# Optimization experiments

Measured on AMD Instinct MI355X. Metric: run time of the kernel, lower is better.

## Reference

```python
import jax, jax.numpy as jnp
import numpy as np

OPTION_NUM = 5
HEADS = 4
NUM_LAYERS = 3
N_NODES = 20000
N_EDGES = 640000
NODES_PER_GRAPH = 800
N_GRAPHS = 25          # N_NODES // NODES_PER_GRAPH, multiple of OPTION_NUM
N_GROUPS = 5           # N_GRAPHS // OPTION_NUM; must equal OPTION_NUM for output_layer
T_TOK = 256
TOKEN_DIM = 1024
D = 256                # out_channels
VOCAB = 100000


def setup_inputs() -> dict:
    key = jax.random.key(0)
    ks = jax.random.split(key, 16)
    nrm = lambda k, s: jax.random.normal(k, s, dtype=jnp.float32) * 0.05
    L = NUM_LAYERS
    return {
        "concept_ids": jax.random.randint(ks[0], (N_NODES,), 0, VOCAB, dtype=jnp.int32),
        "edge_index": jax.random.randint(ks[1], (2, N_EDGES), 0, N_NODES, dtype=jnp.int32),
        "edge_type": jax.random.randint(ks[2], (N_EDGES,), 0, 38, dtype=jnp.int32),
        "sentence_embeddings": nrm(ks[3], (N_GROUPS, TOKEN_DIM)),
        "token_embedding": nrm(ks[4], (N_GROUPS, T_TOK, TOKEN_DIM)),
        "batch": (jnp.arange(N_NODES, dtype=jnp.int32) // NODES_PER_GRAPH),
        "entity_embeddings": nrm(ks[5], (VOCAB, D)),
        "Wq": nrm(ks[6], (L, D, D)), "bq": jnp.zeros((L, D), jnp.float32),
        "Wk": nrm(ks[7], (L, D, D)), "bk": jnp.zeros((L, D), jnp.float32),
        "Wv": nrm(ks[8], (L, D, D)), "bv": jnp.zeros((L, D), jnp.float32),
        "Ws": nrm(ks[9], (L, TOKEN_DIM, D)), "bs": jnp.zeros((L, D), jnp.float32),
        "Wo": nrm(ks[10], (L, D, D)), "bo": jnp.zeros((L, D), jnp.float32),
        "W1": nrm(ks[11], (D, D)), "b1": jnp.zeros((D,), jnp.float32),
        "W2": nrm(ks[12], (TOKEN_DIM, D)), "b2": jnp.zeros((D,), jnp.float32),
        "W3": nrm(ks[13], (D, TOKEN_DIM)), "b3": jnp.zeros((TOKEN_DIM,), jnp.float32),
        "Wout": nrm(ks[14], (OPTION_NUM * D, D)), "bout": jnp.zeros((D,), jnp.float32),
    }


def reference(concept_ids, edge_index, edge_type, sentence_embeddings, token_embedding,
              batch, entity_embeddings, Wq, bq, Wk, bk, Wv, bv, Ws, bs, Wo, bo,
              W1, b1, W2, b2, W3, b3, Wout, bout):
    H = HEADS
    C = D // H
    sqdk = jnp.sqrt(jnp.float32(C))
    group = batch // OPTION_NUM                      # [N] in [0, N_GROUPS)
    row, col = edge_index[0], edge_index[1]

    x = entity_embeddings[concept_ids]               # [N, D]
    for l in range(NUM_LAYERS):
        Q = (x @ Wq[l] + bq[l]).reshape(-1, H, C)
        K = (x @ Wk[l] + bk[l]).reshape(-1, H, C)
        V = (x @ Wv[l] + bv[l]).reshape(-1, H, C)
        QS = (sentence_embeddings[group] @ Ws[l] + bs[l]).reshape(-1, H, C)
        Qi, Kj = Q[row], K[col]                      # [E, H, C]
        alpha = ((Qi * Kj).sum(-1) + (QS[row] * Kj).sum(-1) + (Qi * QS[col]).sum(-1)) / (3.0 * sqdk)
        alpha = jax.nn.leaky_relu(alpha, 0.2)
        alpha = jax.nn.softmax(alpha, axis=0)        # global softmax over edges (as in source)
        agg = jnp.zeros_like(V).at[row].add(V[col] * alpha[:, :, None])
        x = agg.reshape(-1, H * C) @ Wo[l] + bo[l] + x

    x = x @ W1 + b1                                  # [N, D]
    tok = token_embedding @ W2 + b2                  # [G, T, D]

    # attention_multihead (faithful double gather by group indices)
    scale = jnp.sqrt(jnp.float32(D))
    scores = jnp.einsum('nd,btd->bnt', x, tok) / scale   # [G, N, T]
    sel = scores[:, group, :]                            # gather dim 1
    w = jax.nn.softmax(sel, axis=-1)
    ao = jnp.einsum('bnt,btd->bnd', w, tok)              # [G, N, D]
    sel2 = ao[:, group, :]                               # second gather
    concat = jnp.transpose(sel2, (1, 0, 2)).reshape(x.shape[0], -1)  # [N, G*D]
    x = concat @ Wout + bout                             # [N, D]

    pooled = jax.ops.segment_max(x, batch, num_segments=N_GRAPHS)    # global_max_pool
    soft = pooled @ W3 + b3                              # [N_GRAPHS, token_dim]
    return soft.reshape(N_GRAPHS // OPTION_NUM, OPTION_NUM, -1)
```

## Files before the change

### kernel.cpp

```cpp
#include <hip/hip_runtime.h>
#include <hip/hip_bf16.h>

#define NNODES 20000
#define NEDGES 640000
#define DM 256
#define PAD 128

typedef short s16x8 __attribute__((ext_vector_type(8)));
typedef float f32x4 __attribute__((ext_vector_type(4)));
typedef float f32x2 __attribute__((ext_vector_type(2)));

__device__ inline float b2f(unsigned short u) {
  union { unsigned int i; float f; } z;
  z.i = (unsigned int)u << 16;
  return z.f;
}
__device__ inline unsigned short f2b(float f) {
  union { unsigned int i; float f; } z;
  z.f = f;
  unsigned int i = z.i;
  return (unsigned short)((i + 0x7FFFu + ((i >> 16) & 1u)) >> 16);
}

__device__ inline unsigned char f2fp8(float v) {
#if __has_builtin(__builtin_amdgcn_cvt_pk_fp8_f32)
  int t = __builtin_amdgcn_cvt_pk_fp8_f32(v, v, 0, false);
  return (unsigned char)(t & 0xFF);
#else
  union { float f; unsigned int u; } z;
  z.f = v;
  unsigned int s = (z.u >> 31) << 7;
  float av = fabsf(v);
  if (av >= 448.f) return (unsigned char)(s | 0x7E);
  if (av < 0.015625f) {
    int q = (int)rintf(av * 512.f);
    return (unsigned char)(s | (unsigned)q);
  }
  int e32 = (int)((z.u >> 23) & 255) - 127;
  unsigned mant = z.u & 0x7FFFFF;
  unsigned t = mant + 0x7FFFF + ((mant >> 20) & 1);
  if (t >= 0x800000u) { t = 0; e32++; }
  int e4 = e32 + 7;
  unsigned m3 = (t >> 20) & 7;
  if (e4 > 15 || (e4 == 15 && m3 == 7)) return (unsigned char)(s | 0x7E);
  return (unsigned char)(s | (unsigned)((e4 << 3) | m3));
#endif
}

__device__ inline float4 fp8x4_dec(unsigned int u) {
#if __has_builtin(__builtin_amdgcn_cvt_pk_f32_fp8)
  f32x2 lo = __builtin_amdgcn_cvt_pk_f32_fp8((int)u, false);
  f32x2 hi = __builtin_amdgcn_cvt_pk_f32_fp8((int)u, true);
  float4 r;
  r.x = lo[0]; r.y = lo[1]; r.z = hi[0]; r.w = hi[1];
  return r;
#else
  float4 r;
  float* p = &r.x;
#pragma unroll
  for (int j = 0; j < 4; j++) {
    unsigned b = (u >> (8 * j)) & 0xFF;
    unsigned s = b >> 7, e = (b >> 3) & 15, m = b & 7;
    float mag;
    if (e == 0) mag = (float)m * 0.001953125f;
    else {
      union { unsigned int i; float f; } z;
      z.i = ((e + 120u) << 23) | (m << 20);
      mag = z.f;
    }
    p[j] = s ? -mag : mag;
  }
  return r;
#endif
}

__global__ __launch_bounds__(256) void gather_kernel(
    const int* __restrict__ cid, const float* __restrict__ ent,
    float* __restrict__ x, unsigned short* __restrict__ xb, int n) {
  int idx = blockIdx.x * 256 + threadIdx.x;
  if (idx >= n * 64) return;
  int node = idx >> 6, d4 = idx & 63;
  float4 v = reinterpret_cast<const float4*>(ent)[(size_t)cid[node] * 64 + d4];
  reinterpret_cast<float4*>(x)[(size_t)node * 64 + d4] = v;
  ushort4 b;
  b.x = f2b(v.x); b.y = f2b(v.y); b.z = f2b(v.z); b.w = f2b(v.w);
  reinterpret_cast<ushort4*>(xb)[(size_t)node * 64 + d4] = b;
}

__global__ __launch_bounds__(256) void wtrans12_kernel(
    const float* __restrict__ Wq, const float* __restrict__ Wk,
    const float* __restrict__ Wv, const float* __restrict__ Wo,
    unsigned short* __restrict__ WT) {
  int slot = blockIdx.x >> 8;
  int l = slot >> 2, t = slot & 3;
  int n = blockIdx.x & 255;
  int k = threadIdx.x;
  const float* src = (t == 0) ? Wq : (t == 1) ? Wk : (t == 2) ? Wv : Wo;
  WT[(size_t)slot * 65536 + n * 256 + k] =
      f2b(src[(size_t)l * 65536 + k * 256 + n]);
}

__global__ __launch_bounds__(256) void w2t_kernel(const float* __restrict__ W2,
                                                  unsigned short* __restrict__ W2T) {
  int i = blockIdx.x * 256 + threadIdx.x;
  int n = i >> 10, k = i & 1023;
  W2T[n * 1024 + k] = f2b(W2[k * 256 + n]);
}

__global__ __launch_bounds__(256) void tokconv_kernel(
    const float* __restrict__ te, unsigned short* __restrict__ tb) {
  int i = blockIdx.x * 256 + threadIdx.x;
  float4 v = reinterpret_cast<const float4*>(te)[i];
  ushort4 b;
  b.x = f2b(v.x); b.y = f2b(v.y); b.z = f2b(v.z); b.w = f2b(v.w);
  reinterpret_cast<ushort4*>(tb)[i] = b;
}

__global__ __launch_bounds__(256) void fill_kernel(const int* __restrict__ ei,
                                                   const int* __restrict__ batch,
                                                   int* __restrict__ deg,
                                                   int* __restrict__ colPad,
                                                   int E) {
  int e = blockIdx.x * 256 + threadIdx.x;
  if (e >= E) return;
  int r = ei[e];
  int c = ei[E + e];
  int slot = atomicAdd(&deg[r], 1);
  if (slot < PAD) colPad[(size_t)r * PAD + slot] = c | ((batch[c] / 5) << 24);
}

__global__ __launch_bounds__(256) void qs5all_kernel(
    const float* __restrict__ sent, const float* __restrict__ Ws,
    const float* __restrict__ bs, float* __restrict__ QS5all) {
  int g = blockIdx.x, l = blockIdx.y;
  int j = threadIdx.x;
  __shared__ float sh[1024];
  for (int i = j; i < 1024; i += 256) sh[i] = sent[g * 1024 + i];
  __syncthreads();
  const float* W = Ws + (size_t)l * 1024 * 256;
  float acc = bs[l * 256 + j];
  for (int k = 0; k < 1024; k++) acc += sh[k] * W[k * 256 + j];
  QS5all[(size_t)(l * 5 + g) * 256 + j] = acc;
}

__global__ __launch_bounds__(256) void qkv_gemm_kernel(
    const unsigned short* __restrict__ A, const unsigned short* __restrict__ Bt,
    const float* __restrict__ bq, const float* __restrict__ bk,
    const float* __restrict__ bv, float* __restrict__ Qf,
    unsigned char* __restrict__ K8, unsigned char* __restrict__ V8, int M) {
  int wid = threadIdx.x >> 6;
  int lane = threadIdx.x & 63;
  int wr = wid >> 1, wc = wid & 1;
  int rowBase = blockIdx.y * 64 + wr * 32;
  int colBase = blockIdx.x * 64 + wc * 32;
  int r16 = lane & 15, kg = lane >> 4;
  f32x4 acc[2][2] = {};
  for (int k0 = 0; k0 < 256; k0 += 32) {
    s16x8 a[2], b[2];
#pragma unroll
    for (int mi = 0; mi < 2; mi++) {
      int r = rowBase + mi * 16 + r16;
      s16x8 z = {};
      a[mi] = (r < M) ? *reinterpret_cast<const s16x8*>(
                            &A[(size_t)r * 256 + k0 + kg * 8])
                      : z;
    }
#pragma unroll
    for (int ni = 0; ni < 2; ni++) {
      int c = colBase + ni * 16 + r16;
      b[ni] = *reinterpret_cast<const s16x8*>(&Bt[(size_t)c * 256 + k0 + kg * 8]);
    }
#pragma unroll
    for (int mi = 0; mi < 2; mi++)
#pragma unroll
      for (int ni = 0; ni < 2; ni++)
        acc[mi][ni] = __builtin_amdgcn_mfma_f32_16x16x32_bf16(
            a[mi], b[ni], acc[mi][ni], 0, 0, 0);
  }
  int region = (blockIdx.x * 64) >> 8;
  const float* bias = (region == 0) ? bq : (region == 1) ? bk : bv;
  unsigned char* dst8 = (region == 1) ? K8 : V8;
#pragma unroll
  for (int mi = 0; mi < 2; mi++)
#pragma unroll
    for (int ni = 0; ni < 2; ni++) {
      int cg = colBase + ni * 16 + (lane & 15);
      int cr = cg & 255;
      float bia = bias[cr];
#pragma unroll
      for (int reg = 0; reg < 4; reg++) {
        int r = rowBase + mi * 16 + (lane >> 4) * 4 + reg;
        if (r >= M) continue;
        float v = acc[mi][ni][reg] + bia;
        if (region == 0)
          Qf[(size_t)r * 256 + cr] = v;
        else
          dst8[(size_t)r * 256 + cr] = f2fp8(v);
      }
    }
}

__global__ __launch_bounds__(256) void gemm_bf16_kernel(
    const unsigned short* __restrict__ A, const unsigned short* __restrict__ Bt,
    const float* __restrict__ bias, const float* __restrict__ resid,
    float* __restrict__ Cf, unsigned short* __restrict__ Cb, int M, int K) {
  int wid = threadIdx.x >> 6;
  int lane = threadIdx.x & 63;
  int wr = wid >> 1, wc = wid & 1;
  int rowBase = blockIdx.y * 64 + wr * 32;
  int colBase = blockIdx.x * 64 + wc * 32;
  int r16 = lane & 15, kg = lane >> 4;
  f32x4 acc[2][2] = {};
  for (int k0 = 0; k0 < K; k0 += 32) {
    s16x8 a[2], b[2];
#pragma unroll
    for (int mi = 0; mi < 2; mi++) {
      int r = rowBase + mi * 16 + r16;
      s16x8 z = {};
      a[mi] = (r < M) ? *reinterpret_cast<const s16x8*>(
                            &A[(size_t)r * K + k0 + kg * 8])
                      : z;
    }
#pragma unroll
    for (int ni = 0; ni < 2; ni++) {
      int c = colBase + ni * 16 + r16;
      b[ni] = *reinterpret_cast<const s16x8*>(&Bt[(size_t)c * K + k0 + kg * 8]);
    }
#pragma unroll
    for (int mi = 0; mi < 2; mi++)
#pragma unroll
      for (int ni = 0; ni < 2; ni++)
        acc[mi][ni] = __builtin_amdgcn_mfma_f32_16x16x32_bf16(
            a[mi], b[ni], acc[mi][ni], 0, 0, 0);
  }
#pragma unroll
  for (int mi = 0; mi < 2; mi++)
#pragma unroll
    for (int ni = 0; ni < 2; ni++) {
      int c = colBase + ni * 16 + (lane & 15);
      float bia = bias[c];
#pragma unroll
      for (int reg = 0; reg < 4; reg++) {
        int r = rowBase + mi * 16 + (lane >> 4) * 4 + reg;
        if (r >= M) continue;
        float v = acc[mi][ni][reg] + bia;
        if (resid) v += resid[(size_t)r * 256 + c];
        if (Cf) Cf[(size_t)r * 256 + c] = v;
        if (Cb) Cb[(size_t)r * 256 + c] = f2b(v);
      }
    }
}

__global__ __launch_bounds__(256) void rescale_wo_kernel(
    unsigned short* __restrict__ WoT, const float* __restrict__ sums) {
  int i = blockIdx.x * 256 + threadIdx.x;
  int head = (i & 255) >> 6;
  WoT[i] = f2b(b2f(WoT[i]) / sums[head]);
}

template <int DO_AGG>
__global__ __launch_bounds__(256) void fused_edge_kernel(
    const int* __restrict__ deg, const int* __restrict__ colPad,
    const int* __restrict__ batch, const float* __restrict__ Q,
    const unsigned int* __restrict__ K8, const unsigned int* __restrict__ V8,
    const float* __restrict__ QS5, float* __restrict__ sums,
    unsigned short* __restrict__ aggb, int n) {
  int wv = __builtin_amdgcn_readfirstlane(threadIdx.x >> 6);
  int node = blockIdx.x * 4 + wv;
  int lane = threadIdx.x & 63;
  int head = lane >> 4;
  float sum0 = 0.f, sum1 = 0.f, sum2 = 0.f, sum3 = 0.f;
  float4 a0 = {0.f, 0.f, 0.f, 0.f}, a1 = a0, a2 = a0, a3 = a0;
  float4 qe = a0;
  float dq0 = 0.f, dq1 = 0.f, dq2 = 0.f, dq3 = 0.f, dq4 = 0.f;
  int dcount = 0;
  if (node < n) {
    float4 q = reinterpret_cast<const float4*>(Q)[(size_t)node * 64 + lane];
    int gr = batch[node] / 5;
    float4 qs = reinterpret_cast<const float4*>(QS5)[gr * 64 + lane];
    qe.x = q.x + qs.x; qe.y = q.y + qs.y; qe.z = q.z + qs.z; qe.w = q.w + qs.w;
#pragma unroll
    for (int g = 0; g < 5; g++) {
      float4 w = reinterpret_cast<const float4*>(QS5)[g * 64 + lane];
      float d = q.x * w.x + q.y * w.y + q.z * w.z + q.w * w.w;
      d += __shfl_xor(d, 1);
      d += __shfl_xor(d, 2);
      d += __shfl_xor(d, 4);
      d += __shfl_xor(d, 8);
      if (g == 0) dq0 = d;
      else if (g == 1) dq1 = d;
      else if (g == 2) dq2 = d;
      else if (g == 3) dq3 = d;
      else dq4 = d;
    }
    dcount = deg[node];
    if (dcount > PAD) dcount = PAD;
  }
  const int* myCol = colPad + (size_t)node * PAD;
  bool lead = (lane & 15) == 0;
  int m = 0;
  for (; m + 4 <= dcount; m += 4) {
    int cc0 = myCol[m + 0], cc1 = myCol[m + 1];
    int cc2 = myCol[m + 2], cc3 = myCol[m + 3];
    int c0 = cc0 & 0xFFFFFF, c1 = cc1 & 0xFFFFFF;
    int c2 = cc2 & 0xFFFFFF, c3 = cc3 & 0xFFFFFF;
    unsigned int kr0 = K8[(size_t)c0 * 64 + lane];
    unsigned int kr1 = K8[(size_t)c1 * 64 + lane];
    unsigned int kr2 = K8[(size_t)c2 * 64 + lane];
    unsigned int kr3 = K8[(size_t)c3 * 64 + lane];
    unsigned int vr0 = 0, vr1 = 0, vr2 = 0, vr3 = 0;
    if (DO_AGG) {
      vr0 = V8[(size_t)c0 * 64 + lane];
      vr1 = V8[(size_t)c1 * 64 + lane];
      vr2 = V8[(size_t)c2 * 64 + lane];
      vr3 = V8[(size_t)c3 * 64 + lane];
    }
    float4 kd0 = fp8x4_dec(kr0), kd1 = fp8x4_dec(kr1);
    float4 kd2 = fp8x4_dec(kr2), kd3 = fp8x4_dec(kr3);
    float p0 = qe.x * kd0.x + qe.y * kd0.y + qe.z * kd0.z + qe.w * kd0.w;
    float p1 = qe.x * kd1.x + qe.y * kd1.y + qe.z * kd1.z + qe.w * kd1.w;
    float p2 = qe.x * kd2.x + qe.y * kd2.y + qe.z * kd2.z + qe.w * kd2.w;
    float p3 = qe.x * kd3.x + qe.y * kd3.y + qe.z * kd3.z + qe.w * kd3.w;
    p0 += __shfl_xor(p0, 1); p1 += __shfl_xor(p1, 1);
    p2 += __shfl_xor(p2, 1); p3 += __shfl_xor(p3, 1);
    p0 += __shfl_xor(p0, 2); p1 += __shfl_xor(p1, 2);
    p2 += __shfl_xor(p2, 2); p3 += __shfl_xor(p3, 2);
    p0 += __shfl_xor(p0, 4); p1 += __shfl_xor(p1, 4);
    p2 += __shfl_xor(p2, 4); p3 += __shfl_xor(p3, 4);
    p0 += __shfl_xor(p0, 8); p1 += __shfl_xor(p1, 8);
    p2 += __shfl_xor(p2, 8); p3 += __shfl_xor(p3, 8);
    int gc0 = cc0 >> 24, gc1 = cc1 >> 24, gc2 = cc2 >> 24, gc3 = cc3 >> 24;
    float dv0 = (gc0 == 0) ? dq0 : (gc0 == 1) ? dq1 : (gc0 == 2) ? dq2 : (gc0 == 3) ? dq3 : dq4;
    float dv1 = (gc1 == 0) ? dq0 : (gc1 == 1) ? dq1 : (gc1 == 2) ? dq2 : (gc1 == 3) ? dq3 : dq4;
    float dv2 = (gc2 == 0) ? dq0 : (gc2 == 1) ? dq1 : (gc2 == 2) ? dq2 : (gc2 == 3) ? dq3 : dq4;
    float dv3 = (gc3 == 0) ? dq0 : (gc3 == 1) ? dq1 : (gc3 == 2) ? dq2 : (gc3 == 3) ? dq3 : dq4;
    float v0 = (p0 + dv0) * (1.f / 24.f); v0 = (v0 >= 0.f) ? v0 : 0.2f * v0;
    float v1 = (p1 + dv1) * (1.f / 24.f); v1 = (v1 >= 0.f) ? v1 : 0.2f * v1;
    float v2 = (p2 + dv2) * (1.f / 24.f); v2 = (v2 >= 0.f) ? v2 : 0.2f * v2;
    float v3 = (p3 + dv3) * (1.f / 24.f); v3 = (v3 >= 0.f) ? v3 : 0.2f * v3;
    float e0 = __expf(v0), e1 = __expf(v1), e2 = __expf(v2), e3 = __expf(v3);
    if (lead) { sum0 += e0; sum1 += e1; sum2 += e2; sum3 += e3; }
    if (DO_AGG) {
      float4 vd0 = fp8x4_dec(vr0), vd1 = fp8x4_dec(vr1);
      float4 vd2 = fp8x4_dec(vr2), vd3 = fp8x4_dec(vr3);
      a0.x += e0 * vd0.x; a0.y += e0 * vd0.y; a0.z += e0 * vd0.z; a0.w += e0 * vd0.w;
      a1.x += e1 * vd1.x; a1.y += e1 * vd1.y; a1.z += e1 * vd1.z; a1.w += e1 * vd1.w;
      a2.x += e2 * vd2.x; a2.y += e2 * vd2.y; a2.z += e2 * vd2.z; a2.w += e2 * vd2.w;
      a3.x += e3 * vd3.x; a3.y += e3 * vd3.y; a3.z += e3 * vd3.z; a3.w += e3 * vd3.w;
    }
  }
  for (; m < dcount; m++) {
    int cc = myCol[m];
    int c = cc & 0xFFFFFF, gc = cc >> 24;
    float4 kd = fp8x4_dec(K8[(size_t)c * 64 + lane]);
    float p = qe.x * kd.x + qe.y * kd.y + qe.z * kd.z + qe.w * kd.w;
    p += __shfl_xor(p, 1);
    p += __shfl_xor(p, 2);
    p += __shfl_xor(p, 4);
    p += __shfl_xor(p, 8);
    float dqv = (gc == 0) ? dq0 : (gc == 1) ? dq1 : (gc == 2) ? dq2
                : (gc == 3) ? dq3 : dq4;
    float v = (p + dqv) * (1.f / 24.f);
    v = (v >= 0.f) ? v : 0.2f * v;
    float ev = __expf(v);
    if (lead) sum0 += ev;
    if (DO_AGG) {
      float4 vd = fp8x4_dec(V8[(size_t)c * 64 + lane]);
      a0.x += ev * vd.x; a0.y += ev * vd.y; a0.z += ev * vd.z; a0.w += ev * vd.w;
    }
  }
  float sumExp = (sum0 + sum1) + (sum2 + sum3);
  if (DO_AGG && node < n) {
    float4 acc;
    acc.x = (a0.x + a1.x) + (a2.x + a3.x);
    acc.y = (a0.y + a1.y) + (a2.y + a3.y);
    acc.z = (a0.z + a1.z) + (a2.z + a3.z);
    acc.w = (a0.w + a1.w) + (a2.w + a3.w);
    ushort4 b;
    b.x = f2b(acc.x); b.y = f2b(acc.y); b.z = f2b(acc.z); b.w = f2b(acc.w);
    reinterpret_cast<ushort4*>(aggb)[(size_t)node * 64 + lane] = b;
  }
  __shared__ float red[4][4];
  int w = threadIdx.x >> 6;
  if (lead) red[w][head] = sumExp;
  __syncthreads();
  if (threadIdx.x < 4) {
    float t = red[0][threadIdx.x] + red[1][threadIdx.x] + red[2][threadIdx.x] +
              red[3][threadIdx.x];
    atomicAdd(&sums[threadIdx.x], t);
  }
}

__global__ __launch_bounds__(64) void node0_agg_kernel(
    const int* __restrict__ deg, const int* __restrict__ colPad,
    const int* __restrict__ batch, const float* __restrict__ Q,
    const unsigned int* __restrict__ K8, const unsigned int* __restrict__ V8,
    const float* __restrict__ QS5, const float* __restrict__ sums,
    float* __restrict__ agg0) {
  int lane = threadIdx.x;
  int head = lane >> 4;
  float4 q = reinterpret_cast<const float4*>(Q)[lane];
  int gr = batch[0] / 5;
  float4 qs = reinterpret_cast<const float4*>(QS5)[gr * 64 + lane];
  float4 qe = {q.x + qs.x, q.y + qs.y, q.z + qs.z, q.w + qs.w};
  float dq0 = 0.f, dq1 = 0.f, dq2 = 0.f, dq3 = 0.f, dq4 = 0.f;
#pragma unroll
  for (int g = 0; g < 5; g++) {
    float4 w = reinterpret_cast<const float4*>(QS5)[g * 64 + lane];
    float d = q.x * w.x + q.y * w.y + q.z * w.z + q.w * w.w;
    d += __shfl_xor(d, 1);
    d += __shfl_xor(d, 2);
    d += __shfl_xor(d, 4);
    d += __shfl_xor(d, 8);
    if (g == 0) dq0 = d;
    else if (g == 1) dq1 = d;
    else if (g == 2) dq2 = d;
    else if (g == 3) dq3 = d;
    else dq4 = d;
  }
  float4 acc = {0.f, 0.f, 0.f, 0.f};
  int dcount = deg[0];
  if (dcount > PAD) dcount = PAD;
  for (int m = 0; m < dcount; m++) {
    int cc = colPad[m];
    int c = cc & 0xFFFFFF, gc = cc >> 24;
    float4 kd = fp8x4_dec(K8[(size_t)c * 64 + lane]);
    float p = qe.x * kd.x + qe.y * kd.y + qe.z * kd.z + qe.w * kd.w;
    p += __shfl_xor(p, 1);
    p += __shfl_xor(p, 2);
    p += __shfl_xor(p, 4);
    p += __shfl_xor(p, 8);
    float dqv = (gc == 0) ? dq0
                : (gc == 1) ? dq1
                : (gc == 2) ? dq2
                : (gc == 3) ? dq3 : dq4;
    float v = (p + dqv) * (1.f / 24.f);
    v = (v >= 0.f) ? v : 0.2f * v;
    float ev = __expf(v);
    float4 vd = fp8x4_dec(V8[(size_t)c * 64 + lane]);
    acc.x += ev * vd.x;
    acc.y += ev * vd.y;
    acc.z += ev * vd.z;
    acc.w += ev * vd.w;
  }
  float invS = 1.f / sums[head];
  acc.x *= invS; acc.y *= invS; acc.z *= invS; acc.w *= invS;
  reinterpret_cast<float4*>(agg0)[lane] = acc;
}

__global__ __launch_bounds__(1024) void final_head_kernel(
    const float* __restrict__ agg0, const float* __restrict__ Wo2,
    const float* __restrict__ bo2, const float* __restrict__ x,
    const float* __restrict__ W1, const float* __restrict__ b1,
    float* __restrict__ x1) {
  __shared__ float a0[256];
  __shared__ float t1[256];
  __shared__ float part[4][256];
  int tid = threadIdx.x;
  int j = tid & 255, s = tid >> 8;
  if (tid < 256) a0[tid] = agg0[tid];
  __syncthreads();
  float acc = 0.f;
#pragma unroll 8
  for (int k = s * 64; k < s * 64 + 64; k++) acc += a0[k] * Wo2[k * 256 + j];
  part[s][j] = acc;
  __syncthreads();
  if (tid < 256)
    t1[tid] = part[0][tid] + part[1][tid] + part[2][tid] + part[3][tid] +
              bo2[tid] + x[tid];
  __syncthreads();
  float acc2 = 0.f;
#pragma unroll 8
  for (int k = s * 64; k < s * 64 + 64; k++) acc2 += t1[k] * W1[k * 256 + j];
  part[s][j] = acc2;
  __syncthreads();
  if (tid < 256)
    x1[tid] = part[0][tid] + part[1][tid] + part[2][tid] + part[3][tid] +
              b1[tid];
}

__global__ __launch_bounds__(256) void attn_out_kernel(
    const float* __restrict__ x1g, const float* __restrict__ tok,
    float* __restrict__ AO) {
  int b = blockIdx.x;
  int tid = threadIdx.x;
  int wave = tid >> 6, lane = tid & 63;
  int sub = lane >> 4, l16 = lane & 15;
  __shared__ float x1s[256];
  __shared__ float scs[256];
  __shared__ float red[256];
  __shared__ float wgt[256];
  x1s[tid] = x1g[tid];
  __syncthreads();
  const float4* xv4 = reinterpret_cast<const float4*>(x1s);
  for (int it = 0; it < 16; it++) {
    int row = wave * 64 + it * 4 + sub;
    const float4* tr =
        reinterpret_cast<const float4*>(tok + (size_t)(b * 256 + row) * 256);
    float sc = 0.f;
#pragma unroll
    for (int q = 0; q < 4; q++) {
      float4 v = tr[l16 + q * 16];
      float4 xv = xv4[l16 + q * 16];
      sc += v.x * xv.x + v.y * xv.y + v.z * xv.z + v.w * xv.w;
    }
    sc += __shfl_xor(sc, 1);
    sc += __shfl_xor(sc, 2);
    sc += __shfl_xor(sc, 4);
    sc += __shfl_xor(sc, 8);
    if (l16 == 0) scs[row] = sc * (1.f / 16.f);
  }
  __syncthreads();
  float sc = scs[tid];
  red[tid] = sc;
  __syncthreads();
  for (int off = 128; off; off >>= 1) {
    if (tid < off) red[tid] = fmaxf(red[tid], red[tid + off]);
    __syncthreads();
  }
  float mx = red[0];
  __syncthreads();
  float ex = expf(sc - mx);
  red[tid] = ex;
  __syncthreads();
  for (int off = 128; off; off >>= 1) {
    if (tid < off) red[tid] += red[tid + off];
    __syncthreads();
  }
  wgt[tid] = ex / red[0];
  __syncthreads();
  float acc = 0.f;
#pragma unroll 4
  for (int k = 0; k < 256; k++)
    acc += wgt[k] * tok[(size_t)(b * 256 + k) * 256 + tid];
  AO[b * 256 + tid] = acc;
}

__global__ __launch_bounds__(256) void final_y_kernel(
    const float* __restrict__ AO, const float* __restrict__ Wout,
    float* __restrict__ partial) {
  int s = blockIdx.x;
  int j = threadIdx.x;
  __shared__ float a[80];
  if (threadIdx.x < 80) a[threadIdx.x] = AO[s * 80 + threadIdx.x];
  __syncthreads();
  const float* W = Wout + (size_t)s * 80 * 256;
  float acc = 0.f;
#pragma unroll 8
  for (int k = 0; k < 80; k++) acc += a[k] * W[k * 256 + j];
  partial[s * 256 + j] = acc;
}

__global__ __launch_bounds__(256) void final_out2_kernel(
    const float* __restrict__ partial, const float* __restrict__ bout,
    const float* __restrict__ W3, const float* __restrict__ b3,
    float* __restrict__ out) {
  __shared__ float y[256];
  int j = threadIdx.x;
  float acc = bout[j];
#pragma unroll
  for (int s = 0; s < 16; s++) acc += partial[s * 256 + j];
  y[j] = acc;
  __syncthreads();
  int t = blockIdx.x * 256 + j;
  float o = b3[t];
#pragma unroll 8
  for (int k = 0; k < 256; k++) o += y[k] * W3[k * 1024 + t];
  for (int g = 0; g < 25; g++) out[(size_t)g * 1024 + t] = o;
}

extern "C" void kernel_launch(void* const* d_in, const int* in_sizes, int n_in,
                              void* d_out, int out_size, void* d_ws,
                              size_t ws_size, hipStream_t stream) {
  const int* concept_ids = (const int*)d_in[0];
  const int* edge_index = (const int*)d_in[1];
  const float* sent = (const float*)d_in[3];
  const float* tokemb = (const float*)d_in[4];
  const int* batch = (const int*)d_in[5];
  const float* ent = (const float*)d_in[6];
  const float* Wq = (const float*)d_in[7];
  const float* bq = (const float*)d_in[8];
  const float* Wk = (const float*)d_in[9];
  const float* bk = (const float*)d_in[10];
  const float* Wv = (const float*)d_in[11];
  const float* bv = (const float*)d_in[12];
  const float* Ws = (const float*)d_in[13];
  const float* bs = (const float*)d_in[14];
  const float* Wo = (const float*)d_in[15];
  const float* bo = (const float*)d_in[16];
  const float* W1 = (const float*)d_in[17];
  const float* b1 = (const float*)d_in[18];
  const float* W2 = (const float*)d_in[19];
  const float* b2 = (const float*)d_in[20];
  const float* W3 = (const float*)d_in[21];
  const float* b3 = (const float*)d_in[22];
  const float* Wout = (const float*)d_in[23];
  const float* bout = (const float*)d_in[24];
  float* out = (float*)d_out;

  float* ws = (float*)d_ws;
  size_t off_ = 0;
  auto alloc = [&](size_t n) {
    float* p = ws + off_;
    off_ += n;
    return p;
  };
  float* x = alloc((size_t)NNODES * DM);
  float* x2 = alloc((size_t)NNODES * DM);
  float* Qf = alloc((size_t)NNODES * DM);
  unsigned short* xb = (unsigned short*)alloc((size_t)NNODES * DM / 2);
  unsigned short* aggb = (unsigned short*)alloc((size_t)NNODES * DM / 2);
  unsigned char* K8 = (unsigned char*)alloc((size_t)NNODES * DM / 4);
  unsigned char* V8 = (unsigned char*)alloc((size_t)NNODES * DM / 4);
  unsigned short* WT = (unsigned short*)alloc(12 * 65536 / 2);
  unsigned short* W2T = (unsigned short*)alloc(262144 / 2);
  unsigned short* tokb = (unsigned short*)alloc(1280 * 1024 / 2);
  float* tok = alloc(1280 * 256);
  float* QS5all = alloc(3 * 5 * 256);
  float* sums = alloc(16);
  float* agg0 = alloc(256);
  float* x1 = alloc(256);
  float* AO = alloc(1280);
  float* partial = alloc(16 * 256);
  int* deg = (int*)alloc(NNODES);
  int* colPad = (int*)alloc((size_t)NNODES * PAD);

  gather_kernel<<<5000, 256, 0, stream>>>(concept_ids, ent, x, xb, NNODES);
  wtrans12_kernel<<<3072, 256, 0, stream>>>(Wq, Wk, Wv, Wo, WT);
  w2t_kernel<<<1024, 256, 0, stream>>>(W2, W2T);
  tokconv_kernel<<<1280, 256, 0, stream>>>(tokemb, tokb);
  hipMemsetAsync(deg, 0, NNODES * sizeof(int), stream);
  fill_kernel<<<(NEDGES + 255) / 256, 256, 0, stream>>>(edge_index, batch, deg,
                                                        colPad, NEDGES);
  {
    dim3 g(5, 3);
    qs5all_kernel<<<g, 256, 0, stream>>>(sent, Ws, bs, QS5all);
  }
  hipMemsetAsync(sums, 0, 12 * sizeof(float), stream);

  float* xin = x;
  float* xout = x2;
  for (int l = 0; l < 3; l++) {
    unsigned short* WoT = WT + (size_t)(l * 4 + 3) * 65536;
    {
      dim3 g(12, (NNODES + 63) / 64);
      qkv_gemm_kernel<<<g, 256, 0, stream>>>(
          xb, WT + (size_t)(l * 4) * 65536, bq + l * DM, bk + l * DM,
          bv + l * DM, Qf, K8, V8, NNODES);
    }
    if (l < 2) {
      fused_edge_kernel<1><<<5000, 256, 0, stream>>>(
          deg, colPad, batch, Qf, (const unsigned int*)K8,
          (const unsigned int*)V8, QS5all + l * 1280, sums + l * 4, aggb,
          NNODES);
      rescale_wo_kernel<<<256, 256, 0, stream>>>(WoT, sums + l * 4);
      dim3 g(4, (NNODES + 63) / 64);
      gemm_bf16_kernel<<<g, 256, 0, stream>>>(aggb, WoT, bo + l * DM, xin,
                                              xout, xb, NNODES, 256);
      float* tmp = xin;
      xin = xout;
      xout = tmp;
    } else {
      fused_edge_kernel<0><<<5000, 256, 0, stream>>>(
          deg, colPad, batch, Qf, (const unsigned int*)K8,
          (const unsigned int*)V8, QS5all + l * 1280, sums + l * 4, nullptr,
          NNODES);
      node0_agg_kernel<<<1, 64, 0, stream>>>(
          deg, colPad, batch, Qf, (const unsigned int*)K8,
          (const unsigned int*)V8, QS5all + l * 1280, sums + l * 4, agg0);
      final_head_kernel<<<1, 1024, 0, stream>>>(agg0, Wo + (size_t)2 * 65536,
                                                bo + 2 * DM, xin, W1, b1, x1);
    }
  }

  {
    dim3 g(4, 1280 / 64);
    gemm_bf16_kernel<<<g, 256, 0, stream>>>(tokb, W2T, b2, nullptr, tok,
                                            nullptr, 1280, 1024);
  }
  attn_out_kernel<<<5, 256, 0, stream>>>(x1, tok, AO);
  final_y_kernel<<<16, 256, 0, stream>>>(AO, Wout, partial);
  final_out2_kernel<<<4, 256, 0, stream>>>(partial, bout, W3, b3, out);
}
```

Before: 657.8 us.

## Process four edges per wave with 16-byte K/V row loads per lane

Restructures the fused edge kernel so each 64-lane wave splits into four 16-lane groups, each handling a different edge. Each lane now loads a 16-byte uint4 chunk of the FP8 K and V rows instead of a 4-byte word. This cuts the per-edge shuffle reduction from four steps to two, and turns the serial edge loop into parallel edge processing across lane groups. In exchange it adds a cross-group shuffle reduction of 16 accumulators at the end. It also adds masked tail iterations, and lanes in a group sit idle when the degree is not a multiple of four.

```diff
diff --git a/kernel.cpp b/kernel.cpp
--- a/kernel.cpp
+++ b/kernel.cpp
@@ -268,25 +268,42 @@
   int wv = __builtin_amdgcn_readfirstlane(threadIdx.x >> 6);
   int node = blockIdx.x * 4 + wv;
   int lane = threadIdx.x & 63;
-  int head = lane >> 4;
-  float sum0 = 0.f, sum1 = 0.f, sum2 = 0.f, sum3 = 0.f;
-  float4 a0 = {0.f, 0.f, 0.f, 0.f}, a1 = a0, a2 = a0, a3 = a0;
-  float4 qe = a0;
+  int e4 = lane >> 4, l16 = lane & 15;
+  int h = l16 >> 2;
+  const uint4* K4 = reinterpret_cast<const uint4*>(K8);
+  const uint4* V4 = reinterpret_cast<const uint4*>(V8);
+
+  float4 qe0 = {0, 0, 0, 0}, qe1 = qe0, qe2 = qe0, qe3 = qe0;
   float dq0 = 0.f, dq1 = 0.f, dq2 = 0.f, dq3 = 0.f, dq4 = 0.f;
   int dcount = 0;
   if (node < n) {
-    float4 q = reinterpret_cast<const float4*>(Q)[(size_t)node * 64 + lane];
+    const float4* Q4 = reinterpret_cast<const float4*>(Q);
+    const float4* S4 = reinterpret_cast<const float4*>(QS5);
+    float4 qv0 = Q4[(size_t)node * 64 + l16 * 4 + 0];
+    float4 qv1 = Q4[(size_t)node * 64 + l16 * 4 + 1];
+    float4 qv2 = Q4[(size_t)node * 64 + l16 * 4 + 2];
+    float4 qv3 = Q4[(size_t)node * 64 + l16 * 4 + 3];
     int gr = batch[node] / 5;
-    float4 qs = reinterpret_cast<const float4*>(QS5)[gr * 64 + lane];
-    qe.x = q.x + qs.x; qe.y = q.y + qs.y; qe.z = q.z + qs.z; qe.w = q.w + qs.w;
+    float4 s0 = S4[gr * 64 + l16 * 4 + 0];
+    float4 s1 = S4[gr * 64 + l16 * 4 + 1];
+    float4 s2 = S4[gr * 64 + l16 * 4 + 2];
+    float4 s3 = S4[gr * 64 + l16 * 4 + 3];
+    qe0.x = qv0.x + s0.x; qe0.y = qv0.y + s0.y; qe0.z = qv0.z + s0.z; qe0.w = qv0.w + s0.w;
+    qe1.x = qv1.x + s1.x; qe1.y = qv1.y + s1.y; qe1.z = qv1.z + s1.z; qe1.w = qv1.w + s1.w;
+    qe2.x = qv2.x + s2.x; qe2.y = qv2.y + s2.y; qe2.z = qv2.z + s2.z; qe2.w = qv2.w + s2.w;
+    qe3.x = qv3.x + s3.x; qe3.y = qv3.y + s3.y; qe3.z = qv3.z + s3.z; qe3.w = qv3.w + s3.w;
 #pragma unroll
     for (int g = 0; g < 5; g++) {
-      float4 w = reinterpret_cast<const float4*>(QS5)[g * 64 + lane];
-      float d = q.x * w.x + q.y * w.y + q.z * w.z + q.w * w.w;
+      float4 w0 = S4[g * 64 + l16 * 4 + 0];
+      float4 w1 = S4[g * 64 + l16 * 4 + 1];
+      float4 w2 = S4[g * 64 + l16 * 4 + 2];
+      float4 w3 = S4[g * 64 + l16 * 4 + 3];
+      float d = qv0.x * w0.x + qv0.y * w0.y + qv0.z * w0.z + qv0.w * w0.w +
+                qv1.x * w1.x + qv1.y * w1.y + qv1.z * w1.z + qv1.w * w1.w +
+                qv2.x * w2.x + qv2.y * w2.y + qv2.z * w2.z + qv2.w * w2.w +
+                qv3.x * w3.x + qv3.y * w3.y + qv3.z * w3.z + qv3.w * w3.w;
       d += __shfl_xor(d, 1);
       d += __shfl_xor(d, 2);
-      d += __shfl_xor(d, 4);
-      d += __shfl_xor(d, 8);
       if (g == 0) dq0 = d;
       else if (g == 1) dq1 = d;
       else if (g == 2) dq2 = d;
@@ -297,92 +314,94 @@
     if (dcount > PAD) dcount = PAD;
   }
   const int* myCol = colPad + (size_t)node * PAD;
-  bool lead = (lane & 15) == 0;
+  float sumExp = 0.f;
+  float4 ac0 = {0, 0, 0, 0}, ac1 = ac0, ac2 = ac0, ac3 = ac0;
+  bool lead = (l16 & 3) == 0;
+
+#define EDGE4(MBASE, MASKED)                                                   \
+  {                                                                            \
+    int idx = (MBASE) + e4;                                                    \
+    bool valid = MASKED ? (idx < dcount) : true;                               \
+    int cc = valid ? myCol[idx] : 0;                                           \
+    int c = cc & 0xFFFFFF, gc = cc >> 24;                                      \
+    uint4 kr = K4[(size_t)c * 16 + l16];                                       \
+    uint4 vr = {0, 0, 0, 0};                                                   \
+    if (DO_AGG) vr = V4[(size_t)c * 16 + l16];                                 \
+    float4 kd0 = fp8x4_dec(kr.x), kd1 = fp8x4_dec(kr.y);                       \
+    float4 kd2 = fp8x4_dec(kr.z), kd3 = fp8x4_dec(kr.w);                       \
+    float p0 = qe0.x * kd0.x + qe0.y * kd0.y + qe0.z * kd0.z + qe0.w * kd0.w;  \
+    float p1 = qe1.x * kd1.x + qe1.y * kd1.y + qe1.z * kd1.z + qe1.w * kd1.w;  \
+    float p2 = qe2.x * kd2.x + qe2.y * kd2.y + qe2.z * kd2.z + qe2.w * kd2.w;  \
+    float p3 = qe3.x * kd3.x + qe3.y * kd3.y + qe3.z * kd3.z + qe3.w * kd3.w;  \
+    float p = (p0 + p1) + (p2 + p3);                                           \
+    p += __shfl_xor(p, 1);                                                     \
+    p += __shfl_xor(p, 2);                                                     \
+    float dv = (gc == 0) ? dq0 : (gc == 1) ? dq1 : (gc == 2) ? dq2             \
+               : (gc == 3) ? dq3 : dq4;                                        \
+    float sv = (p + dv) * (1.f / 24.f);                                        \
+    sv = (sv >= 0.f) ? sv : 0.2f * sv;                                         \
+    float ev = __expf(sv);                                                     \
+    if (MASKED && !valid) ev = 0.f;                                            \
+    if (lead) sumExp += ev;                                                    \
+    if (DO_AGG) {                                                              \
+      float4 vd0 = fp8x4_dec(vr.x), vd1 = fp8x4_dec(vr.y);                     \
+      float4 vd2 = fp8x4_dec(vr.z), vd3 = fp8x4_dec(vr.w);                     \
+      ac0.x += ev * vd0.x; ac0.y += ev * vd0.y; ac0.z += ev * vd0.z;           \
+      ac0.w += ev * vd0.w;                                                     \
+      ac1.x += ev * vd1.x; ac1.y += ev * vd1.y; ac1.z += ev * vd1.z;           \
+      ac1.w += ev * vd1.w;                                                     \
+      ac2.x += ev * vd2.x; ac2.y += ev * vd2.y; ac2.z += ev * vd2.z;           \
+      ac2.w += ev * vd2.w;                                                     \
+      ac3.x += ev * vd3.x; ac3.y += ev * vd3.y; ac3.z += ev * vd3.z;           \
+      ac3.w += ev * vd3.w;                                                     \
+    }                                                                          \
+  }
+
   int m = 0;
-  for (; m + 4 <= dcount; m += 4) {
-    int cc0 = myCol[m + 0], cc1 = myCol[m + 1];
-    int cc2 = myCol[m + 2], cc3 = myCol[m + 3];
-    int c0 = cc0 & 0xFFFFFF, c1 = cc1 & 0xFFFFFF;
-    int c2 = cc2 & 0xFFFFFF, c3 = cc3 & 0xFFFFFF;
-    unsigned int kr0 = K8[(size_t)c0 * 64 + lane];
-    unsigned int kr1 = K8[(size_t)c1 * 64 + lane];
-    unsigned int kr2 = K8[(size_t)c2 * 64 + lane];
-    unsigned int kr3 = K8[(size_t)c3 * 64 + lane];
-    unsigned int vr0 = 0, vr1 = 0, vr2 = 0, vr3 = 0;
-    if (DO_AGG) {
-      vr0 = V8[(size_t)c0 * 64 + lane];
-      vr1 = V8[(size_t)c1 * 64 + lane];
-      vr2 = V8[(size_t)c2 * 64 + lane];
-      vr3 = V8[(size_t)c3 * 64 + lane];
-    }
-    float4 kd0 = fp8x4_dec(kr0), kd1 = fp8x4_dec(kr1);
-    float4 kd2 = fp8x4_dec(kr2), kd3 = fp8x4_dec(kr3);
-    float p0 = qe.x * kd0.x + qe.y * kd0.y + qe.z * kd0.z + qe.w * kd0.w;
-    float p1 = qe.x * kd1.x + qe.y * kd1.y + qe.z * kd1.z + qe.w * kd1.w;
-    float p2 = qe.x * kd2.x + qe.y * kd2.y + qe.z * kd2.z + qe.w * kd2.w;
-    float p3 = qe.x * kd3.x + qe.y * kd3.y + qe.z * kd3.z + qe.w * kd3.w;
-    p0 += __shfl_xor(p0, 1); p1 += __shfl_xor(p1, 1);
-    p2 += __shfl_xor(p2, 1); p3 += __shfl_xor(p3, 1);
-    p0 += __shfl_xor(p0, 2); p1 += __shfl_xor(p1, 2);
-    p2 += __shfl_xor(p2, 2); p3 += __shfl_xor(p3, 2);
-    p0 += __shfl_xor(p0, 4); p1 += __shfl_xor(p1, 4);
-    p2 += __shfl_xor(p2, 4); p3 += __shfl_xor(p3, 4);
-    p0 += __shfl_xor(p0, 8); p1 += __shfl_xor(p1, 8);
-    p2 += __shfl_xor(p2, 8); p3 += __shfl_xor(p3, 8);
-    int gc0 = cc0 >> 24, gc1 = cc1 >> 24, gc2 = cc2 >> 24, gc3 = cc3 >> 24;
-    float dv0 = (gc0 == 0) ? dq0 : (gc0 == 1) ? dq1 : (gc0 == 2) ? dq2 : (gc0 == 3) ? dq3 : dq4;
-    float dv1 = (gc1 == 0) ? dq0 : (gc1 == 1) ? dq1 : (gc1 == 2) ? dq2 : (gc1 == 3) ? dq3 : dq4;
-    float dv2 = (gc2 == 0) ? dq0 : (gc2 == 1) ? dq1 : (gc2 == 2) ? dq2 : (gc2 == 3) ? dq3 : dq4;
-    float dv3 = (gc3 == 0) ? dq0 : (gc3 == 1) ? dq1 : (gc3 == 2) ? dq2 : (gc3 == 3) ? dq3 : dq4;
-    float v0 = (p0 + dv0) * (1.f / 24.f); v0 = (v0 >= 0.f) ? v0 : 0.2f * v0;
-    float v1 = (p1 + dv1) * (1.f / 24.f); v1 = (v1 >= 0.f) ? v1 : 0.2f * v1;
-    float v2 = (p2 + dv2) * (1.f / 24.f); v2 = (v2 >= 0.f) ? v2 : 0.2f * v2;
-    float v3 = (p3 + dv3) * (1.f / 24.f); v3 = (v3 >= 0.f) ? v3 : 0.2f * v3;
-    float e0 = __expf(v0), e1 = __expf(v1), e2 = __expf(v2), e3 = __expf(v3);
-    if (lead) { sum0 += e0; sum1 += e1; sum2 += e2; sum3 += e3; }
-    if (DO_AGG) {
-      float4 vd0 = fp8x4_dec(vr0), vd1 = fp8x4_dec(vr1);
-      float4 vd2 = fp8x4_dec(vr2), vd3 = fp8x4_dec(vr3);
-      a0.x += e0 * vd0.x; a0.y += e0 * vd0.y; a0.z += e0 * vd0.z; a0.w += e0 * vd0.w;
-      a1.x += e1 * vd1.x; a1.y += e1 * vd1.y; a1.z += e1 * vd1.z; a1.w += e1 * vd1.w;
-      a2.x += e2 * vd2.x; a2.y += e2 * vd2.y; a2.z += e2 * vd2.z; a2.w += e2 * vd2.w;
-      a3.x += e3 * vd3.x; a3.y += e3 * vd3.y; a3.z += e3 * vd3.z; a3.w += e3 * vd3.w;
-    }
-  }
-  for (; m < dcount; m++) {
-    int cc = myCol[m];
-    int c = cc & 0xFFFFFF, gc = cc >> 24;
-    float4 kd = fp8x4_dec(K8[(size_t)c * 64 + lane]);
-    float p = qe.x * kd.x + qe.y * kd.y + qe.z * kd.z + qe.w * kd.w;
-    p += __shfl_xor(p, 1);
-    p += __shfl_xor(p, 2);
-    p += __shfl_xor(p, 4);
-    p += __shfl_xor(p, 8);
-    float dqv = (gc == 0) ? dq0 : (gc == 1) ? dq1 : (gc == 2) ? dq2
-                : (gc == 3) ? dq3 : dq4;
-    float v = (p + dqv) * (1.f / 24.f);
-    v = (v >= 0.f) ? v : 0.2f * v;
-    float ev = __expf(v);
-    if (lead) sum0 += ev;
-    if (DO_AGG) {
-      float4 vd = fp8x4_dec(V8[(size_t)c * 64 + lane]);
-      a0.x += ev * vd.x; a0.y += ev * vd.y; a0.z += ev * vd.z; a0.w += ev * vd.w;
-    }
-  }
-  float sumExp = (sum0 + sum1) + (sum2 + sum3);
+  for (; m + 8 <= dcount; m += 8) {
+    EDGE4(m, false)
+    EDGE4(m + 4, false)
+  }
+  for (; m < dcount; m += 4) {
+    EDGE4(m, true)
+  }
+#undef EDGE4
+
+  sumExp += __shfl_xor(sumExp, 16);
+  sumExp += __shfl_xor(sumExp, 32);
   if (DO_AGG && node < n) {
-    float4 acc;
-    acc.x = (a0.x + a1.x) + (a2.x + a3.x);
-    acc.y = (a0.y + a1.y) + (a2.y + a3.y);
-    acc.z = (a0.z + a1.z) + (a2.z + a3.z);
-    acc.w = (a0.w + a1.w) + (a2.w + a3.w);
-    ushort4 b;
-    b.x = f2b(acc.x); b.y = f2b(acc.y); b.z = f2b(acc.z); b.w = f2b(acc.w);
-    reinterpret_cast<ushort4*>(aggb)[(size_t)node * 64 + lane] = b;
+    ac0.x += __shfl_xor(ac0.x, 16); ac0.x += __shfl_xor(ac0.x, 32);
+    ac0.y += __shfl_xor(ac0.y, 16); ac0.y += __shfl_xor(ac0.y, 32);
+    ac0.z += __shfl_xor(ac0.z, 16); ac0.z += __shfl_xor(ac0.z, 32);
+    ac0.w += __shfl_xor(ac0.w, 16); ac0.w += __shfl_xor(ac0.w, 32);
+    ac1.x += __shfl_xor(ac1.x, 16); ac1.x += __shfl_xor(ac1.x, 32);
+    ac1.y += __shfl_xor(ac1.y, 16); ac1.y += __shfl_xor(ac1.y, 32);
+    ac1.z += __shfl_xor(ac1.z, 16); ac1.z += __shfl_xor(ac1.z, 32);
+    ac1.w += __shfl_xor(ac1.w, 16); ac1.w += __shfl_xor(ac1.w, 32);
+    ac2.x += __shfl_xor(ac2.x, 16); ac2.x += __shfl_xor(ac2.x, 32);
+    ac2.y += __shfl_xor(ac2.y, 16); ac2.y += __shfl_xor(ac2.y, 32);
+    ac2.z += __shfl_xor(ac2.z, 16); ac2.z += __shfl_xor(ac2.z, 32);
+    ac2.w += __shfl_xor(ac2.w, 16); ac2.w += __shfl_xor(ac2.w, 32);
+    ac3.x += __shfl_xor(ac3.x, 16); ac3.x += __shfl_xor(ac3.x, 32);
+    ac3.y += __shfl_xor(ac3.y, 16); ac3.y += __shfl_xor(ac3.y, 32);
+    ac3.z += __shfl_xor(ac3.z, 16); ac3.z += __shfl_xor(ac3.z, 32);
+    ac3.w += __shfl_xor(ac3.w, 16); ac3.w += __shfl_xor(ac3.w, 32);
+    if (e4 == 0) {
+      ushort4* A4 = reinterpret_cast<ushort4*>(aggb);
+      ushort4 b0, b1, b2, b3;
+      b0.x = f2b(ac0.x); b0.y = f2b(ac0.y); b0.z = f2b(ac0.z); b0.w = f2b(ac0.w);
+      b1.x = f2b(ac1.x); b1.y = f2b(ac1.y); b1.z = f2b(ac1.z); b1.w = f2b(ac1.w);
+      b2.x = f2b(ac2.x); b2.y = f2b(ac2.y); b2.z = f2b(ac2.z); b2.w = f2b(ac2.w);
+      b3.x = f2b(ac3.x); b3.y = f2b(ac3.y); b3.z = f2b(ac3.z); b3.w = f2b(ac3.w);
+      A4[(size_t)node * 64 + l16 * 4 + 0] = b0;
+      A4[(size_t)node * 64 + l16 * 4 + 1] = b1;
+      A4[(size_t)node * 64 + l16 * 4 + 2] = b2;
+      A4[(size_t)node * 64 + l16 * 4 + 3] = b3;
+    }
   }
   __shared__ float red[4][4];
   int w = threadIdx.x >> 6;
-  if (lead) red[w][head] = sumExp;
+  if (e4 == 0 && lead) red[w][h] = sumExp;
   __syncthreads();
   if (threadIdx.x < 4) {
     float t = red[0][threadIdx.x] + red[1][threadIdx.x] + red[2][threadIdx.x] +
```

Result: slower. 674.9 us (+2.6%).

## Split each node's edge list across two wavefronts in fused edge kernel

Applied to the files above, without the earlier changes.

Each destination node is now handled by two wavefronts that take alternating groups of four edges. Their partial aggregates are combined through shared memory before the bf16 store, and the grid doubles to 10000 blocks. The remainder loop is replaced by a single masked four-edge step. The aim is to expose more memory-level parallelism for the gather-bound K/V loads, at the cost of duplicated per-node setup work (Q load, dot products with QS5) and an extra shared-memory combine.

```diff
diff --git a/kernel.cpp b/kernel.cpp
--- a/kernel.cpp
+++ b/kernel.cpp
@@ -266,7 +266,8 @@
     const float* __restrict__ QS5, float* __restrict__ sums,
     unsigned short* __restrict__ aggb, int n) {
   int wv = __builtin_amdgcn_readfirstlane(threadIdx.x >> 6);
-  int node = blockIdx.x * 4 + wv;
+  int node = blockIdx.x * 2 + (wv >> 1);
+  int half = wv & 1;
   int lane = threadIdx.x & 63;
   int head = lane >> 4;
   float sum0 = 0.f, sum1 = 0.f, sum2 = 0.f, sum3 = 0.f;
@@ -298,92 +299,113 @@
   }
   const int* myCol = colPad + (size_t)node * PAD;
   bool lead = (lane & 15) == 0;
-  int m = 0;
-  for (; m + 4 <= dcount; m += 4) {
-    int cc0 = myCol[m + 0], cc1 = myCol[m + 1];
-    int cc2 = myCol[m + 2], cc3 = myCol[m + 3];
-    int c0 = cc0 & 0xFFFFFF, c1 = cc1 & 0xFFFFFF;
-    int c2 = cc2 & 0xFFFFFF, c3 = cc3 & 0xFFFFFF;
-    unsigned int kr0 = K8[(size_t)c0 * 64 + lane];
-    unsigned int kr1 = K8[(size_t)c1 * 64 + lane];
-    unsigned int kr2 = K8[(size_t)c2 * 64 + lane];
-    unsigned int kr3 = K8[(size_t)c3 * 64 + lane];
-    unsigned int vr0 = 0, vr1 = 0, vr2 = 0, vr3 = 0;
-    if (DO_AGG) {
-      vr0 = V8[(size_t)c0 * 64 + lane];
-      vr1 = V8[(size_t)c1 * 64 + lane];
-      vr2 = V8[(size_t)c2 * 64 + lane];
-      vr3 = V8[(size_t)c3 * 64 + lane];
-    }
-    float4 kd0 = fp8x4_dec(kr0), kd1 = fp8x4_dec(kr1);
-    float4 kd2 = fp8x4_dec(kr2), kd3 = fp8x4_dec(kr3);
-    float p0 = qe.x * kd0.x + qe.y * kd0.y + qe.z * kd0.z + qe.w * kd0.w;
-    float p1 = qe.x * kd1.x + qe.y * kd1.y + qe.z * kd1.z + qe.w * kd1.w;
-    float p2 = qe.x * kd2.x + qe.y * kd2.y + qe.z * kd2.z + qe.w * kd2.w;
-    float p3 = qe.x * kd3.x + qe.y * kd3.y + qe.z * kd3.z + qe.w * kd3.w;
-    p0 += __shfl_xor(p0, 1); p1 += __shfl_xor(p1, 1);
-    p2 += __shfl_xor(p2, 1); p3 += __shfl_xor(p3, 1);
-    p0 += __shfl_xor(p0, 2); p1 += __shfl_xor(p1, 2);
-    p2 += __shfl_xor(p2, 2); p3 += __shfl_xor(p3, 2);
-    p0 += __shfl_xor(p0, 4); p1 += __shfl_xor(p1, 4);
-    p2 += __shfl_xor(p2, 4); p3 += __shfl_xor(p3, 4);
-    p0 += __shfl_xor(p0, 8); p1 += __shfl_xor(p1, 8);
-    p2 += __shfl_xor(p2, 8); p3 += __shfl_xor(p3, 8);
-    int gc0 = cc0 >> 24, gc1 = cc1 >> 24, gc2 = cc2 >> 24, gc3 = cc3 >> 24;
-    float dv0 = (gc0 == 0) ? dq0 : (gc0 == 1) ? dq1 : (gc0 == 2) ? dq2 : (gc0 == 3) ? dq3 : dq4;
-    float dv1 = (gc1 == 0) ? dq0 : (gc1 == 1) ? dq1 : (gc1 == 2) ? dq2 : (gc1 == 3) ? dq3 : dq4;
-    float dv2 = (gc2 == 0) ? dq0 : (gc2 == 1) ? dq1 : (gc2 == 2) ? dq2 : (gc2 == 3) ? dq3 : dq4;
-    float dv3 = (gc3 == 0) ? dq0 : (gc3 == 1) ? dq1 : (gc3 == 2) ? dq2 : (gc3 == 3) ? dq3 : dq4;
-    float v0 = (p0 + dv0) * (1.f / 24.f); v0 = (v0 >= 0.f) ? v0 : 0.2f * v0;
-    float v1 = (p1 + dv1) * (1.f / 24.f); v1 = (v1 >= 0.f) ? v1 : 0.2f * v1;
-    float v2 = (p2 + dv2) * (1.f / 24.f); v2 = (v2 >= 0.f) ? v2 : 0.2f * v2;
-    float v3 = (p3 + dv3) * (1.f / 24.f); v3 = (v3 >= 0.f) ? v3 : 0.2f * v3;
-    float e0 = __expf(v0), e1 = __expf(v1), e2 = __expf(v2), e3 = __expf(v3);
-    if (lead) { sum0 += e0; sum1 += e1; sum2 += e2; sum3 += e3; }
-    if (DO_AGG) {
-      float4 vd0 = fp8x4_dec(vr0), vd1 = fp8x4_dec(vr1);
-      float4 vd2 = fp8x4_dec(vr2), vd3 = fp8x4_dec(vr3);
-      a0.x += e0 * vd0.x; a0.y += e0 * vd0.y; a0.z += e0 * vd0.z; a0.w += e0 * vd0.w;
-      a1.x += e1 * vd1.x; a1.y += e1 * vd1.y; a1.z += e1 * vd1.z; a1.w += e1 * vd1.w;
-      a2.x += e2 * vd2.x; a2.y += e2 * vd2.y; a2.z += e2 * vd2.z; a2.w += e2 * vd2.w;
-      a3.x += e3 * vd3.x; a3.y += e3 * vd3.y; a3.z += e3 * vd3.z; a3.w += e3 * vd3.w;
-    }
-  }
-  for (; m < dcount; m++) {
-    int cc = myCol[m];
-    int c = cc & 0xFFFFFF, gc = cc >> 24;
-    float4 kd = fp8x4_dec(K8[(size_t)c * 64 + lane]);
-    float p = qe.x * kd.x + qe.y * kd.y + qe.z * kd.z + qe.w * kd.w;
-    p += __shfl_xor(p, 1);
-    p += __shfl_xor(p, 2);
-    p += __shfl_xor(p, 4);
-    p += __shfl_xor(p, 8);
-    float dqv = (gc == 0) ? dq0 : (gc == 1) ? dq1 : (gc == 2) ? dq2
-                : (gc == 3) ? dq3 : dq4;
-    float v = (p + dqv) * (1.f / 24.f);
-    v = (v >= 0.f) ? v : 0.2f * v;
-    float ev = __expf(v);
-    if (lead) sum0 += ev;
-    if (DO_AGG) {
-      float4 vd = fp8x4_dec(V8[(size_t)c * 64 + lane]);
-      a0.x += ev * vd.x; a0.y += ev * vd.y; a0.z += ev * vd.z; a0.w += ev * vd.w;
-    }
-  }
+
+#define EDGE4(MBASE, MASKED)                                                   \
+  {                                                                            \
+    int i0 = (MBASE), i1 = (MBASE) + 1, i2 = (MBASE) + 2, i3 = (MBASE) + 3;    \
+    bool v0_ = MASKED ? (i0 < dcount) : true;                                  \
+    bool v1_ = MASKED ? (i1 < dcount) : true;                                  \
+    bool v2_ = MASKED ? (i2 < dcount) : true;                                  \
+    bool v3_ = MASKED ? (i3 < dcount) : true;                                  \
+    int cc0 = v0_ ? myCol[i0] : 0;                                             \
+    int cc1 = v1_ ? myCol[i1] : 0;                                             \
+    int cc2 = v2_ ? myCol[i2] : 0;                                             \
+    int cc3 = v3_ ? myCol[i3] : 0;                                             \
+    int c0 = cc0 & 0xFFFFFF, c1 = cc1 & 0xFFFFFF;                              \
+    int c2 = cc2 & 0xFFFFFF, c3 = cc3 & 0xFFFFFF;                              \
+    unsigned int kr0 = K8[(size_t)c0 * 64 + lane];                             \
+    unsigned int kr1 = K8[(size_t)c1 * 64 + lane];                             \
+    unsigned int kr2 = K8[(size_t)c2 * 64 + lane];                             \
+    unsigned int kr3 = K8[(size_t)c3 * 64 + lane];                             \
+    unsigned int vr0 = 0, vr1 = 0, vr2 = 0, vr3 = 0;                           \
+    if (DO_AGG) {                                                              \
+      vr0 = V8[(size_t)c0 * 64 + lane];                                        \
+      vr1 = V8[(size_t)c1 * 64 + lane];                                        \
+      vr2 = V8[(size_t)c2 * 64 + lane];                                        \
+      vr3 = V8[(size_t)c3 * 64 + lane];                                        \
+    }                                                                          \
+    float4 kd0 = fp8x4_dec(kr0), kd1 = fp8x4_dec(kr1);                         \
+    float4 kd2 = fp8x4_dec(kr2), kd3 = fp8x4_dec(kr3);                         \
+    float p0 = qe.x * kd0.x + qe.y * kd0.y + qe.z * kd0.z + qe.w * kd0.w;      \
+    float p1 = qe.x * kd1.x + qe.y * kd1.y + qe.z * kd1.z + qe.w * kd1.w;      \
+    float p2 = qe.x * kd2.x + qe.y * kd2.y + qe.z * kd2.z + qe.w * kd2.w;      \
+    float p3 = qe.x * kd3.x + qe.y * kd3.y + qe.z * kd3.z + qe.w * kd3.w;      \
+    p0 += __shfl_xor(p0, 1); p1 += __shfl_xor(p1, 1);                          \
+    p2 += __shfl_xor(p2, 1); p3 += __shfl_xor(p3, 1);                          \
+    p0 += __shfl_xor(p0, 2); p1 += __shfl_xor(p1, 2);                          \
+    p2 += __shfl_xor(p2, 2); p3 += __shfl_xor(p3, 2);                          \
+    p0 += __shfl_xor(p0, 4); p1 += __shfl_xor(p1, 4);                          \
+    p2 += __shfl_xor(p2, 4); p3 += __shfl_xor(p3, 4);                          \
+    p0 += __shfl_xor(p0, 8); p1 += __shfl_xor(p1, 8);                          \
+    p2 += __shfl_xor(p2, 8); p3 += __shfl_xor(p3, 8);                          \
+    int gc0 = cc0 >> 24, gc1 = cc1 >> 24, gc2 = cc2 >> 24, gc3 = cc3 >> 24;    \
+    float dv0 = (gc0 == 0) ? dq0 : (gc0 == 1) ? dq1 : (gc0 == 2) ? dq2         \
+                : (gc0 == 3) ? dq3 : dq4;                                      \
+    float dv1 = (gc1 == 0) ? dq0 : (gc1 == 1) ? dq1 : (gc1 == 2) ? dq2         \
+                : (gc1 == 3) ? dq3 : dq4;                                      \
+    float dv2 = (gc2 == 0) ? dq0 : (gc2 == 1) ? dq1 : (gc2 == 2) ? dq2         \
+                : (gc2 == 3) ? dq3 : dq4;                                      \
+    float dv3 = (gc3 == 0) ? dq0 : (gc3 == 1) ? dq1 : (gc3 == 2) ? dq2         \
+                : (gc3 == 3) ? dq3 : dq4;                                      \
+    float s0_ = (p0 + dv0) * (1.f / 24.f); s0_ = (s0_ >= 0.f) ? s0_ : 0.2f * s0_; \
+    float s1_ = (p1 + dv1) * (1.f / 24.f); s1_ = (s1_ >= 0.f) ? s1_ : 0.2f * s1_; \
+    float s2_ = (p2 + dv2) * (1.f / 24.f); s2_ = (s2_ >= 0.f) ? s2_ : 0.2f * s2_; \
+    float s3_ = (p3 + dv3) * (1.f / 24.f); s3_ = (s3_ >= 0.f) ? s3_ : 0.2f * s3_; \
+    float e0 = __expf(s0_), e1 = __expf(s1_), e2 = __expf(s2_), e3 = __expf(s3_); \
+    if (MASKED) {                                                              \
+      if (!v0_) e0 = 0.f;                                                      \
+      if (!v1_) e1 = 0.f;                                                      \
+      if (!v2_) e2 = 0.f;                                                      \
+      if (!v3_) e3 = 0.f;                                                      \
+    }                                                                          \
+    if (lead) { sum0 += e0; sum1 += e1; sum2 += e2; sum3 += e3; }              \
+    if (DO_AGG) {                                                              \
+      float4 vd0 = fp8x4_dec(vr0), vd1 = fp8x4_dec(vr1);                       \
+      float4 vd2 = fp8x4_dec(vr2), vd3 = fp8x4_dec(vr3);                       \
+      a0.x += e0 * vd0.x; a0.y += e0 * vd0.y; a0.z += e0 * vd0.z;              \
+      a0.w += e0 * vd0.w;                                                      \
+      a1.x += e1 * vd1.x; a1.y += e1 * vd1.y; a1.z += e1 * vd1.z;              \
+      a1.w += e1 * vd1.w;                                                      \
+      a2.x += e2 * vd2.x; a2.y += e2 * vd2.y; a2.z += e2 * vd2.z;              \
+      a2.w += e2 * vd2.w;                                                      \
+      a3.x += e3 * vd3.x; a3.y += e3 * vd3.y; a3.z += e3 * vd3.z;              \
+      a3.w += e3 * vd3.w;                                                      \
+    }                                                                          \
+  }
+
+  int m = half * 4;
+  for (; m + 4 <= dcount; m += 8) {
+    EDGE4(m, false)
+  }
+  if (m < dcount) {
+    EDGE4(m, true)
+  }
+#undef EDGE4
+
   float sumExp = (sum0 + sum1) + (sum2 + sum3);
-  if (DO_AGG && node < n) {
+  __shared__ float4 lacc[4][64];
+  if (DO_AGG) {
     float4 acc;
     acc.x = (a0.x + a1.x) + (a2.x + a3.x);
     acc.y = (a0.y + a1.y) + (a2.y + a3.y);
     acc.z = (a0.z + a1.z) + (a2.z + a3.z);
     acc.w = (a0.w + a1.w) + (a2.w + a3.w);
-    ushort4 b;
-    b.x = f2b(acc.x); b.y = f2b(acc.y); b.z = f2b(acc.z); b.w = f2b(acc.w);
-    reinterpret_cast<ushort4*>(aggb)[(size_t)node * 64 + lane] = b;
+    lacc[wv][lane] = acc;
   }
   __shared__ float red[4][4];
   int w = threadIdx.x >> 6;
   if (lead) red[w][head] = sumExp;
   __syncthreads();
+  if (DO_AGG && half == 0 && node < n) {
+    float4 mine = lacc[wv][lane];
+    float4 other = lacc[wv + 1][lane];
+    ushort4 b;
+    b.x = f2b(mine.x + other.x);
+    b.y = f2b(mine.y + other.y);
+    b.z = f2b(mine.z + other.z);
+    b.w = f2b(mine.w + other.w);
+    reinterpret_cast<ushort4*>(aggb)[(size_t)node * 64 + lane] = b;
+  }
   if (threadIdx.x < 4) {
     float t = red[0][threadIdx.x] + red[1][threadIdx.x] + red[2][threadIdx.x] +
               red[3][threadIdx.x];
@@ -649,7 +671,7 @@
           bv + l * DM, Qf, K8, V8, NNODES);
     }
     if (l < 2) {
-      fused_edge_kernel<1><<<5000, 256, 0, stream>>>(
+      fused_edge_kernel<1><<<10000, 256, 0, stream>>>(
           deg, colPad, batch, Qf, (const unsigned int*)K8,
           (const unsigned int*)V8, QS5all + l * 1280, sums + l * 4, aggb,
           NNODES);
@@ -661,7 +683,7 @@
       xin = xout;
       xout = tmp;
     } else {
-      fused_edge_kernel<0><<<5000, 256, 0, stream>>>(
+      fused_edge_kernel<0><<<10000, 256, 0, stream>>>(
           deg, colPad, batch, Qf, (const unsigned int*)K8,
           (const unsigned int*)V8, QS5all + l * 1280, sums + l * 4, nullptr,
           NNODES);
```

After: 822.7 us. +25.1%, slower.
